# Kernel tuning notes

Hardware: AMD Instinct MI355X
Metric: run time of the kernel (lower is better)

Reference implementation:

```python
import jax, jax.numpy as jnp
import numpy as np

NUM_EXPERTS = 8
IN_FEATURES = 1024
OUT_FEATURES = 1024
TOTAL_TOKENS = 8192


def setup_inputs() -> dict:
    key = jax.random.key(0)
    k_x, k_w, k_b = jax.random.split(key, 3)
    inputs = jax.random.normal(k_x, (TOTAL_TOKENS, IN_FEATURES), dtype=jnp.float32)
    # lecun_normal-style scale for the per-expert kernels
    kernel = jax.random.normal(k_w, (NUM_EXPERTS, IN_FEATURES, OUT_FEATURES), dtype=jnp.float32) / np.sqrt(IN_FEATURES)
    bias = jax.random.normal(k_b, (NUM_EXPERTS, OUT_FEATURES), dtype=jnp.float32) * 0.01
    # ragged group sizes that sum exactly to TOTAL_TOKENS (tokens pre-sorted by expert)
    rng = np.random.default_rng(0)
    gs = rng.multinomial(TOTAL_TOKENS, [1.0 / NUM_EXPERTS] * NUM_EXPERTS)
    group_sizes = jnp.asarray(gs, dtype=jnp.int32)
    return {"inputs": inputs, "group_sizes": group_sizes, "kernel": kernel, "bias": bias}


def reference(inputs, group_sizes, kernel, bias):
    # inputs: [T, in], kernel: [E, in, out], bias: [E, out], group_sizes: [E]
    E = kernel.shape[0]
    T = inputs.shape[0]
    # per-token expert id (tokens are sorted/grouped by expert)
    expert_ids = jnp.repeat(jnp.arange(E, dtype=jnp.int32), group_sizes, total_repeat_length=T)  # [T]
    onehot = jax.nn.one_hot(expert_ids, E, dtype=inputs.dtype)  # [T, E]
    # grouped ragged matmul: y[t] = x[t] @ W[expert_ids[t]]
    xe = jnp.einsum("te,ti->eti", onehot, inputs)  # [E, T, in], zero outside each expert's group
    y = jnp.einsum("eti,eio->to", xe, kernel)  # [T, out]
    # ragged bias expansion: bias of the owning expert per token
    y = y + jnp.take(bias, expert_ids, axis=0)
    return y
```

## Files before the change

kernel.cpp:

```cpp
#include <hip/hip_runtime.h>
#include <hip/hip_bf16.h>

#define KDIM 1024
#define NDIM 1024
#define NEXP 8
#define TTOK 8192
#define LDA  40

typedef __bf16 bf16x8 __attribute__((ext_vector_type(8)));
typedef __bf16 bf16x4 __attribute__((ext_vector_type(4)));
typedef float  f32x4  __attribute__((ext_vector_type(4)));

__device__ __forceinline__ void gl2lds16(const void* g, void* l) {
  __builtin_amdgcn_global_load_lds(
      (const __attribute__((address_space(1))) void*)g,
      (__attribute__((address_space(3))) void*)l, 16, 0, 0);
}

__global__ __launch_bounds__(256) void prepass(
    const float* __restrict__ x, const float* __restrict__ W,
    __bf16* __restrict__ xb, __bf16* __restrict__ Wt)
{
  __shared__ __align__(16) __bf16 Lt[64 * 72];
  const int t = threadIdx.x;
  if (blockIdx.x < 1024) {
    int gid = blockIdx.x * 256 + t;
#pragma unroll
    for (int p = 0; p < 4; ++p) {
      size_t i8 = (size_t)(gid + p * 262144) * 8;
      float4 a = *(const float4*)(x + i8);
      float4 b = *(const float4*)(x + i8 + 4);
      bf16x8 v;
      v[0] = (__bf16)a.x; v[1] = (__bf16)a.y; v[2] = (__bf16)a.z; v[3] = (__bf16)a.w;
      v[4] = (__bf16)b.x; v[5] = (__bf16)b.y; v[6] = (__bf16)b.z; v[7] = (__bf16)b.w;
      *(bf16x8*)(xb + i8) = v;
    }
  } else {
    int bid = blockIdx.x - 1024;
    int e = bid >> 8, r = bid & 255;
    int k0 = (r >> 4) * 64, n0 = (r & 15) * 64;
    const float* Wp = W + (size_t)e * KDIM * NDIM;
    int rr0 = t >> 4, c4 = t & 15;
#pragma unroll
    for (int p = 0; p < 4; ++p) {
      int kk = rr0 + p * 16;
      float4 v = *(const float4*)(Wp + (size_t)(k0 + kk) * NDIM + n0 + c4 * 4);
      Lt[(c4 * 4 + 0) * 72 + kk] = (__bf16)v.x;
      Lt[(c4 * 4 + 1) * 72 + kk] = (__bf16)v.y;
      Lt[(c4 * 4 + 2) * 72 + kk] = (__bf16)v.z;
      Lt[(c4 * 4 + 3) * 72 + kk] = (__bf16)v.w;
    }
    __syncthreads();
    __bf16* Wte = Wt + (size_t)e * NDIM * KDIM;
    int n = t >> 2, kq = t & 3;
#pragma unroll
    for (int q = 0; q < 2; ++q) {
      int kqq = kq + q * 4;
      bf16x8 v = *(const bf16x8*)(Lt + n * 72 + kqq * 8);
      *(bf16x8*)(Wte + (size_t)(n0 + n) * KDIM + k0 + kqq * 8) = v;
    }
  }
}

__global__ __launch_bounds__(256) void moe_gemm_bf16(
    const __bf16* __restrict__ xb, const __bf16* __restrict__ Wt,
    const int* __restrict__ gs, const float* __restrict__ bias,
    float* __restrict__ out)
{
  __shared__ __align__(16) __bf16 Al[4096];
  __shared__ __align__(16) __bf16 Bl[4096];

  int y = blockIdx.y;
  int e = 0, row0 = 0, rows = 0, found = 0, off = 0;
#pragma unroll
  for (int i = 0; i < NEXP; ++i) {
    int g = gs[i];
    int tc = (g + 127) >> 7;
    if (!found) {
      if (y < tc) { found = 1; e = i; row0 = off + y * 128; rows = min(128, g - y * 128); }
      else y -= tc;
    }
    off += g;
  }
  if (!found) return;
  const int n0 = blockIdx.x * 128;

  const int t = threadIdx.x, lane = t & 63, wv = t >> 6;
  const int wm = wv & 1, wn = wv >> 1, lm = lane & 15, lg = lane >> 4;

  const int c0 = wv * 2, c1 = wv * 2 + 1;
  const int s0 = c0 * 64 + lane, s1 = c1 * 64 + lane;
  const int r0 = s0 & 127, k0h = s0 >> 7;
  const int r1 = s1 & 127, k1h = s1 >> 7;

  const __bf16* gA0 = xb + (size_t)(row0 + r0) * KDIM + k0h * 8;
  const __bf16* gA1 = xb + (size_t)(row0 + r1) * KDIM + k1h * 8;
  const __bf16* Wte = Wt + (size_t)e * NDIM * KDIM;
  const __bf16* gB0 = Wte + (size_t)(n0 + r0) * KDIM + k0h * 8;
  const __bf16* gB1 = Wte + (size_t)(n0 + r1) * KDIM + k1h * 8;
  __bf16* lA0 = Al + c0 * 512;
  __bf16* lA1 = Al + c1 * 512;
  __bf16* lB0 = Bl + c0 * 512;
  __bf16* lB1 = Bl + c1 * 512;

  f32x4 acc[4][4] = {};

#pragma unroll 1
  for (int kt = 0; kt < KDIM / 32; ++kt) {
    const int ko = kt * 32;
    gl2lds16(gA0 + ko, lA0);
    gl2lds16(gA1 + ko, lA1);
    gl2lds16(gB0 + ko, lB0);
    gl2lds16(gB1 + ko, lB1);
    __syncthreads();

    bf16x8 af[4], bfr[4];
#pragma unroll
    for (int i = 0; i < 4; ++i)
      af[i] = *(const bf16x8*)(Al + lg * 1024 + (wm * 64 + i * 16 + lm) * 8);
#pragma unroll
    for (int j = 0; j < 4; ++j)
      bfr[j] = *(const bf16x8*)(Bl + lg * 1024 + (wn * 64 + j * 16 + lm) * 8);

#pragma unroll
    for (int i = 0; i < 4; ++i)
#pragma unroll
      for (int j = 0; j < 4; ++j)
        acc[i][j] = __builtin_amdgcn_mfma_f32_16x16x32_bf16(af[i], bfr[j], acc[i][j], 0, 0, 0);
    __syncthreads();
  }

  float bj[4];
#pragma unroll
  for (int j = 0; j < 4; ++j) bj[j] = bias[e * NDIM + n0 + wn * 64 + j * 16 + lm];
  float* op = out + (size_t)row0 * NDIM + n0;
#pragma unroll
  for (int i = 0; i < 4; ++i)
#pragma unroll
    for (int r = 0; r < 4; ++r) {
      int rr = wm * 64 + i * 16 + lg * 4 + r;
      if (rr < rows) {
#pragma unroll
        for (int j = 0; j < 4; ++j)
          op[(size_t)rr * NDIM + wn * 64 + j * 16 + lm] = acc[i][j][r] + bj[j];
      }
    }
}

__global__ __launch_bounds__(256) void moe_gemm_kernel(
    const float* __restrict__ x, const int* __restrict__ gs,
    const float* __restrict__ W, const float* __restrict__ bias,
    float* __restrict__ out)
{
  __shared__ __bf16 Al[128 * LDA];
  __shared__ __bf16 Bl[128 * LDA];
  const int e = blockIdx.z, mt = blockIdx.y, nt = blockIdx.x;
  int off = 0;
#pragma unroll
  for (int i = 0; i < NEXP; ++i) { int g = gs[i]; if (i < e) off += g; }
  const int ge = gs[e];
  const int m0 = mt * 128;
  if (m0 >= ge) return;
  const int rows = min(128, ge - m0);
  const int row0 = off + m0;
  const int n0 = nt * 128;
  const int t = threadIdx.x, lane = t & 63, wv = t >> 6;
  const int wm = wv & 1, wn = wv >> 1, lm = lane & 15, lg = lane >> 4;
  const int am = t >> 3, kq = t & 7, nb = t & 127, kh = t >> 7;
  float4 aReg[4]; float bReg[16];
  const float* Wp = W + (size_t)e * KDIM * NDIM + n0 + nb;
  auto load_tile = [&](int kt) {
#pragma unroll
    for (int p = 0; p < 4; ++p) {
      int r = am + 32 * p;
      if (r < rows) aReg[p] = *(const float4*)(x + (size_t)(row0 + r) * KDIM + kt * 32 + kq * 4);
      else aReg[p] = make_float4(0.f, 0.f, 0.f, 0.f);
    }
    const float* wp = Wp + (size_t)(kt * 32 + kh * 16) * NDIM;
#pragma unroll
    for (int j = 0; j < 16; ++j) bReg[j] = wp[(size_t)j * NDIM];
  };
  auto store_tile = [&]() {
#pragma unroll
    for (int p = 0; p < 4; ++p) {
      bf16x4 v;
      v[0] = (__bf16)aReg[p].x; v[1] = (__bf16)aReg[p].y;
      v[2] = (__bf16)aReg[p].z; v[3] = (__bf16)aReg[p].w;
      *(bf16x4*)(Al + (am + 32 * p) * LDA + kq * 4) = v;
    }
    bf16x8 b0, b1;
#pragma unroll
    for (int j = 0; j < 8; ++j) { b0[j] = (__bf16)bReg[j]; b1[j] = (__bf16)bReg[8 + j]; }
    *(bf16x8*)(Bl + nb * LDA + kh * 16) = b0;
    *(bf16x8*)(Bl + nb * LDA + kh * 16 + 8) = b1;
  };
  f32x4 acc[4][4] = {};
  load_tile(0);
#pragma unroll 1
  for (int kt = 0; kt < KDIM / 32; ++kt) {
    __syncthreads();
    store_tile();
    __syncthreads();
    if (kt + 1 < KDIM / 32) load_tile(kt + 1);
    bf16x8 af[4], bfr[4];
#pragma unroll
    for (int i = 0; i < 4; ++i)
      af[i] = *(const bf16x8*)(Al + (wm * 64 + i * 16 + lm) * LDA + lg * 8);
#pragma unroll
    for (int j = 0; j < 4; ++j)
      bfr[j] = *(const bf16x8*)(Bl + (wn * 64 + j * 16 + lm) * LDA + lg * 8);
#pragma unroll
    for (int i = 0; i < 4; ++i)
#pragma unroll
      for (int j = 0; j < 4; ++j)
        acc[i][j] = __builtin_amdgcn_mfma_f32_16x16x32_bf16(af[i], bfr[j], acc[i][j], 0, 0, 0);
  }
  float bj[4];
#pragma unroll
  for (int j = 0; j < 4; ++j) bj[j] = bias[e * NDIM + n0 + wn * 64 + j * 16 + lm];
  float* op = out + (size_t)row0 * NDIM + n0;
#pragma unroll
  for (int i = 0; i < 4; ++i)
#pragma unroll
    for (int r = 0; r < 4; ++r) {
      int rr = wm * 64 + i * 16 + lg * 4 + r;
      if (rr < rows) {
#pragma unroll
        for (int j = 0; j < 4; ++j)
          op[(size_t)rr * NDIM + wn * 64 + j * 16 + lm] = acc[i][j][r] + bj[j];
      }
    }
}

extern "C" void kernel_launch(void* const* d_in, const int* in_sizes, int n_in,
                              void* d_out, int out_size, void* d_ws, size_t ws_size,
                              hipStream_t stream) {
  const float* x    = (const float*)d_in[0];
  const int*   gs   = (const int*)d_in[1];
  const float* W    = (const float*)d_in[2];
  const float* bias = (const float*)d_in[3];
  float*       out  = (float*)d_out;

  const size_t xb_bytes = (size_t)TTOK * KDIM * 2;
  const size_t wt_bytes = (size_t)NEXP * KDIM * NDIM * 2;
  if (ws_size >= xb_bytes + wt_bytes) {
    __bf16* xb = (__bf16*)d_ws;
    __bf16* Wt = (__bf16*)((char*)d_ws + xb_bytes);
    prepass<<<dim3(1024 + 2048), 256, 0, stream>>>(x, W, xb, Wt);
    moe_gemm_bf16<<<dim3(NDIM / 128, 72), 256, 0, stream>>>(xb, Wt, gs, bias, out);
  } else {
    moe_gemm_kernel<<<dim3(NDIM / 128, TTOK / 128, NEXP), 256, 0, stream>>>(x, gs, W, bias, out);
  }
}
```

Baseline: 161.5 us.

## Double-buffer LDS tiles in bf16 MoE GEMM to overlap loads with MFMA

Doubles the shared-memory A/B tiles in the bf16 grouped GEMM and restructures the K loop into a two-stage ping-pong. While one buffer is consumed by the MFMA work, the async global-to-LDS loads for the next K tile are already in flight. This hides global load latency, which was previously fully exposed by a load-then-barrier-then-compute pattern. The cost is twice the LDS footprint per block, which may reduce occupancy, and a dependency on barriers draining the async LDS loads.

```diff
diff --git a/kernel.cpp b/kernel.cpp
--- a/kernel.cpp
+++ b/kernel.cpp
@@ -5,7 +5,6 @@
 #define NDIM 1024
 #define NEXP 8
 #define TTOK 8192
-#define LDA  40
 
 typedef __bf16 bf16x8 __attribute__((ext_vector_type(8)));
 typedef __bf16 bf16x4 __attribute__((ext_vector_type(4)));
@@ -67,8 +66,8 @@
     const int* __restrict__ gs, const float* __restrict__ bias,
     float* __restrict__ out)
 {
-  __shared__ __align__(16) __bf16 Al[4096];
-  __shared__ __align__(16) __bf16 Bl[4096];
+  __shared__ __align__(16) __bf16 Al0[4096], Bl0[4096];
+  __shared__ __align__(16) __bf16 Al1[4096], Bl1[4096];
 
   int y = blockIdx.y;
   int e = 0, row0 = 0, rows = 0, found = 0, off = 0;
@@ -98,36 +97,41 @@
   const __bf16* Wte = Wt + (size_t)e * NDIM * KDIM;
   const __bf16* gB0 = Wte + (size_t)(n0 + r0) * KDIM + k0h * 8;
   const __bf16* gB1 = Wte + (size_t)(n0 + r1) * KDIM + k1h * 8;
-  __bf16* lA0 = Al + c0 * 512;
-  __bf16* lA1 = Al + c1 * 512;
-  __bf16* lB0 = Bl + c0 * 512;
-  __bf16* lB1 = Bl + c1 * 512;
 
   f32x4 acc[4][4] = {};
 
-#pragma unroll 1
-  for (int kt = 0; kt < KDIM / 32; ++kt) {
+  auto stage = [&](int kt, __bf16* lA, __bf16* lB) {
     const int ko = kt * 32;
-    gl2lds16(gA0 + ko, lA0);
-    gl2lds16(gA1 + ko, lA1);
-    gl2lds16(gB0 + ko, lB0);
-    gl2lds16(gB1 + ko, lB1);
-    __syncthreads();
-
+    gl2lds16(gA0 + ko, lA + c0 * 512);
+    gl2lds16(gA1 + ko, lA + c1 * 512);
+    gl2lds16(gB0 + ko, lB + c0 * 512);
+    gl2lds16(gB1 + ko, lB + c1 * 512);
+  };
+
+  auto compute = [&](const __bf16* lA, const __bf16* lB) {
     bf16x8 af[4], bfr[4];
 #pragma unroll
     for (int i = 0; i < 4; ++i)
-      af[i] = *(const bf16x8*)(Al + lg * 1024 + (wm * 64 + i * 16 + lm) * 8);
+      af[i] = *(const bf16x8*)(lA + lg * 1024 + (wm * 64 + i * 16 + lm) * 8);
 #pragma unroll
     for (int j = 0; j < 4; ++j)
-      bfr[j] = *(const bf16x8*)(Bl + lg * 1024 + (wn * 64 + j * 16 + lm) * 8);
-
+      bfr[j] = *(const bf16x8*)(lB + lg * 1024 + (wn * 64 + j * 16 + lm) * 8);
 #pragma unroll
     for (int i = 0; i < 4; ++i)
 #pragma unroll
       for (int j = 0; j < 4; ++j)
         acc[i][j] = __builtin_amdgcn_mfma_f32_16x16x32_bf16(af[i], bfr[j], acc[i][j], 0, 0, 0);
-    __syncthreads();
+  };
+
+  stage(0, Al0, Bl0);
+#pragma unroll 1
+  for (int kt = 0; kt < KDIM / 32; kt += 2) {
+    __syncthreads();
+    stage(kt + 1, Al1, Bl1);
+    compute(Al0, Bl0);
+    __syncthreads();
+    if (kt + 2 < KDIM / 32) stage(kt + 2, Al0, Bl0);
+    compute(Al1, Bl1);
   }
 
   float bj[4];
@@ -147,6 +151,7 @@
     }
 }
 
+#define LDA 40
 __global__ __launch_bounds__(256) void moe_gemm_kernel(
     const float* __restrict__ x, const int* __restrict__ gs,
     const float* __restrict__ W, const float* __restrict__ bias,
```

New measurement: 164.4 us. About the same (+1.8%).
